# Kernel optimization log

Hardware: AMD Instinct MI355X
Metric: run time of the kernel (lower is better)

Reference implementation:

```python
import jax, jax.numpy as jnp
import numpy as np

N_USER = 100000
N_ITEM = 200000
N_NODES = N_USER + N_ITEM
NNZ = 4000000
EMB = 64
N_LAYERS = 3
BATCH = 4096


def setup_inputs() -> dict:
    key = jax.random.key(0)
    ks = jax.random.split(key, 12)
    inp = {
        'users': jax.random.randint(ks[0], (BATCH,), 0, N_USER, dtype=jnp.int32),
        'pos_items': jax.random.randint(ks[1], (BATCH,), 0, N_ITEM, dtype=jnp.int32),
        'neg_items': jax.random.randint(ks[2], (BATCH,), 0, N_ITEM, dtype=jnp.int32),
        'row': jax.random.randint(ks[3], (NNZ,), 0, N_NODES, dtype=jnp.int32),
        'col': jax.random.randint(ks[4], (NNZ,), 0, N_NODES, dtype=jnp.int32),
        'vals': jax.random.uniform(ks[5], (NNZ,), dtype=jnp.float32),
        'user_emb': 0.1 * jax.random.normal(ks[6], (N_USER, EMB), dtype=jnp.float32),
        'item_emb': 0.1 * jax.random.normal(ks[7], (N_ITEM, EMB), dtype=jnp.float32),
        'W_gc': 0.1 * jax.random.normal(ks[8], (N_LAYERS, EMB, EMB), dtype=jnp.float32),
        'b_gc': 0.1 * jax.random.normal(ks[9], (N_LAYERS, EMB), dtype=jnp.float32),
        'W_bi': 0.1 * jax.random.normal(ks[10], (N_LAYERS, EMB, EMB), dtype=jnp.float32),
        'b_bi': 0.1 * jax.random.normal(ks[11], (N_LAYERS, EMB), dtype=jnp.float32),
    }
    return inp


def _l2_normalize(x, eps=1e-12):
    # matches torch F.normalize(p=2, dim=1): x / max(||x||, eps)
    n = jnp.sqrt(jnp.sum(x * x, axis=1, keepdims=True))
    return x / jnp.maximum(n, eps)


def reference(users, pos_items, neg_items, row, col, vals, user_emb, item_emb, W_gc, b_gc, W_bi, b_bi):
    B = users.shape[0]
    # sparse adjacency propagation: side = A_hat @ [user_emb; item_emb]
    emb = jnp.concatenate([user_emb, item_emb], axis=0)          # [N, d]
    msgs = vals[:, None] * emb[col]                               # [nnz, d]
    side = jax.ops.segment_sum(msgs, row, num_segments=N_NODES)  # [N, d]

    u_side = side[users]                                          # [B, d]
    i_side = jnp.concatenate([side[N_USER + pos_items], side[N_USER + neg_items]], axis=0)
    small_side = jnp.concatenate([u_side, i_side], axis=0)        # [3B, d]
    ego = jnp.concatenate([user_emb[users], item_emb[pos_items], item_emb[neg_items]], axis=0)

    all_embeddings = [ego]
    for k in range(N_LAYERS):
        sum_e = small_side @ W_gc[k] + b_gc[k]
        bi = (ego * small_side) @ W_bi[k] + b_bi[k]
        ego = jax.nn.leaky_relu(sum_e + bi, negative_slope=0.2)
        all_embeddings.append(_l2_normalize(ego))

    all_e = jnp.concatenate(all_embeddings, axis=1)               # [3B, d*(L+1)]
    u_g = all_e[:B]
    i_g = all_e[B:]
    pos_g = i_g[:B]
    neg_g = i_g[B:]
    return (u_g, pos_g, neg_g)
```

## Files before the change

kernel.cpp:

```cpp
#include <hip/hip_runtime.h>

#define N_USER   100000
#define N_ITEM   200000
#define N_NODES  300000
#define NNZ      4000000
#define EMB      64
#define N_LAYERS 3
#define BATCH    4096
#define NSLOT    (3*BATCH)
#define MAXE     96


__global__ void k_setup(const int* __restrict__ users,
                        const int* __restrict__ pos,
                        const int* __restrict__ neg,
                        int* __restrict__ slot_of_node,
                        int* __restrict__ count) {
    int i = blockIdx.x * blockDim.x + threadIdx.x;
    if (i >= NSLOT) return;
    count[i] = 0;
    int node;
    if (i < BATCH)            node = users[i];
    else if (i < 2 * BATCH)   node = N_USER + pos[i - BATCH];
    else                      node = N_USER + neg[i - 2 * BATCH];
    slot_of_node[node] = i;
}

__global__ void __launch_bounds__(256) k_build(
        const int* __restrict__ row,
        const int* __restrict__ col,
        const float* __restrict__ vals,
        const int* __restrict__ slot_of_node,
        int* __restrict__ count,
        int* __restrict__ csr_col,
        float* __restrict__ csr_val) {
    int stride = gridDim.x * blockDim.x;
    for (int e = blockIdx.x * blockDim.x + threadIdx.x; e < NNZ; e += stride) {
        int s = slot_of_node[row[e]];
        if (s >= 0) {
            int p = atomicAdd(&count[s], 1);
            if (p < MAXE) {
                csr_col[(size_t)s * MAXE + p] = col[e];
                csr_val[(size_t)s * MAXE + p] = vals[e];
            }
        }
    }
}

__global__ void __launch_bounds__(256) k_gather_mlp(
        const int* __restrict__ users,
        const int* __restrict__ pos,
        const int* __restrict__ neg,
        const float* __restrict__ user_emb,
        const float* __restrict__ item_emb,
        const float* __restrict__ W_gc,
        const float* __restrict__ b_gc,
        const float* __restrict__ W_bi,
        const float* __restrict__ b_bi,
        const int* __restrict__ slot_of_node,
        const int* __restrict__ count,
        const int* __restrict__ csr_col,
        const float* __restrict__ csr_val,
        float* __restrict__ out) {
    __shared__ float s_lds[4][EMB];
    __shared__ float e_lds[4][EMB];
    int w = threadIdx.x >> 6;
    int j = threadIdx.x & 63;
    int slot = blockIdx.x * 4 + w;

    int node;
    if (slot < BATCH)          node = users[slot];
    else if (slot < 2 * BATCH) node = N_USER + pos[slot - BATCH];
    else                       node = N_USER + neg[slot - 2 * BATCH];

    const float* erow = (node < N_USER) ? (user_emb + (size_t)node * EMB)
                                        : (item_emb + (size_t)(node - N_USER) * EMB);
    int wslot = slot_of_node[node];
    int n = count[wslot];
    n = (n < MAXE) ? n : MAXE;
    const int*   cc = csr_col + (size_t)wslot * MAXE;
    const float* cv = csr_val + (size_t)wslot * MAXE;

    float acc = 0.f;
    int t = 0;
    for (; t + 1 < n; t += 2) {
        int   c0 = cc[t],     c1 = cc[t + 1];
        float v0 = cv[t],     v1 = cv[t + 1];
        const float* s0 = (c0 < N_USER) ? (user_emb + (size_t)c0 * EMB)
                                        : (item_emb + (size_t)(c0 - N_USER) * EMB);
        const float* s1 = (c1 < N_USER) ? (user_emb + (size_t)c1 * EMB)
                                        : (item_emb + (size_t)(c1 - N_USER) * EMB);
        float g0 = s0[j];
        float g1 = s1[j];
        acc = fmaf(v0, g0, acc);
        acc = fmaf(v1, g1, acc);
    }
    if (t < n) {
        int   c0 = cc[t];
        float v0 = cv[t];
        const float* s0 = (c0 < N_USER) ? (user_emb + (size_t)c0 * EMB)
                                        : (item_emb + (size_t)(c0 - N_USER) * EMB);
        acc = fmaf(v0, s0[j], acc);
    }

    float e0 = erow[j];
    s_lds[w][j] = acc;
    e_lds[w][j] = e0;
    out[(size_t)slot * 256 + j] = e0;
    __syncthreads();

    for (int k = 0; k < N_LAYERS; ++k) {
        const float* wgc = W_gc + (size_t)k * EMB * EMB;
        const float* wbi = W_bi + (size_t)k * EMB * EMB;
        float sum1 = b_gc[k * EMB + j];
        float sum2 = b_bi[k * EMB + j];
        #pragma unroll 8
        for (int i = 0; i < EMB; ++i) {
            float si = s_lds[w][i];
            float pi = si * e_lds[w][i];
            sum1 = fmaf(si, wgc[i * EMB + j], sum1);
            sum2 = fmaf(pi, wbi[i * EMB + j], sum2);
        }
        float x = sum1 + sum2;
        x = (x >= 0.f) ? x : 0.2f * x;

        float sq = x * x;
        #pragma unroll
        for (int o = 32; o; o >>= 1) sq += __shfl_xor(sq, o, 64);
        float nn = fmaxf(sqrtf(sq), 1e-12f);
        out[(size_t)slot * 256 + (k + 1) * 64 + j] = x / nn;

        __syncthreads();
        e_lds[w][j] = x;
        __syncthreads();
    }
}

extern "C" void kernel_launch(void* const* d_in, const int* in_sizes, int n_in,
                              void* d_out, int out_size, void* d_ws, size_t ws_size,
                              hipStream_t stream) {
    const int*   users    = (const int*)  d_in[0];
    const int*   pos      = (const int*)  d_in[1];
    const int*   neg      = (const int*)  d_in[2];
    const int*   row      = (const int*)  d_in[3];
    const int*   col      = (const int*)  d_in[4];
    const float* vals     = (const float*)d_in[5];
    const float* user_emb = (const float*)d_in[6];
    const float* item_emb = (const float*)d_in[7];
    const float* W_gc     = (const float*)d_in[8];
    const float* b_gc     = (const float*)d_in[9];
    const float* W_bi     = (const float*)d_in[10];
    const float* b_bi     = (const float*)d_in[11];
    float* out = (float*)d_out;

    char* ws = (char*)d_ws;
    int*   slot_of_node = (int*)ws;
    int*   count        = (int*)(ws + 1200128);
    int*   csr_col      = (int*)(ws + 1249280);
    float* csr_val      = (float*)(ws + 5967872);

    hipMemsetAsync(slot_of_node, 0xFF, (size_t)N_NODES * sizeof(int), stream);

    k_setup<<<(NSLOT + 255) / 256, 256, 0, stream>>>(users, pos, neg,
                                                     slot_of_node, count);
    k_build<<<2048, 256, 0, stream>>>(row, col, vals, slot_of_node,
                                      count, csr_col, csr_val);
    k_gather_mlp<<<NSLOT / 4, 256, 0, stream>>>(users, pos, neg,
                                                user_emb, item_emb,
                                                W_gc, b_gc, W_bi, b_bi,
                                                slot_of_node, count,
                                                csr_col, csr_val, out);
}
```

Before: 92.15 us.

## Vectorize edge scan, stage MLP weights in LDS, batch neighbor gathers via shuffles

The build kernel now reads row indices as int4 with one thread per four edges, replacing the grid-stride loop. The gather/MLP kernel uses 512-thread blocks (8 slots each), loads each layer's W_gc and W_bi into shared memory, and broadcasts the per-slot vectors with wave shuffles instead of LDS arrays. Neighbor indices and values are fetched once per lane and broadcast by shuffle, with 16 gathers issued before their FMAs to expose memory-level parallelism. The risk is the per-layer weight reload and the block-wide syncs that add latency and LDS pressure (32KB per block), which may lower occupancy.

```diff
diff --git a/kernel.cpp b/kernel.cpp
--- a/kernel.cpp
+++ b/kernel.cpp
@@ -9,6 +9,8 @@
 #define BATCH    4096
 #define NSLOT    (3*BATCH)
 #define MAXE     96
+#define BDIM     512
+#define WPB      8
 
 
 __global__ void k_setup(const int* __restrict__ users,
@@ -34,20 +36,21 @@
         int* __restrict__ count,
         int* __restrict__ csr_col,
         float* __restrict__ csr_val) {
-    int stride = gridDim.x * blockDim.x;
-    for (int e = blockIdx.x * blockDim.x + threadIdx.x; e < NNZ; e += stride) {
-        int s = slot_of_node[row[e]];
-        if (s >= 0) {
-            int p = atomicAdd(&count[s], 1);
-            if (p < MAXE) {
-                csr_col[(size_t)s * MAXE + p] = col[e];
-                csr_val[(size_t)s * MAXE + p] = vals[e];
-            }
-        }
-    }
+    int t = blockIdx.x * blockDim.x + threadIdx.x;
+    if (t >= NNZ / 4) return;
+    int4 r = ((const int4*)row)[t];
+    int s0 = slot_of_node[r.x];
+    int s1 = slot_of_node[r.y];
+    int s2 = slot_of_node[r.z];
+    int s3 = slot_of_node[r.w];
+    int e = t * 4;
+    if (s0 >= 0) { int p = atomicAdd(&count[s0], 1); if (p < MAXE) { csr_col[(size_t)s0*MAXE+p] = col[e];   csr_val[(size_t)s0*MAXE+p] = vals[e];   } }
+    if (s1 >= 0) { int p = atomicAdd(&count[s1], 1); if (p < MAXE) { csr_col[(size_t)s1*MAXE+p] = col[e+1]; csr_val[(size_t)s1*MAXE+p] = vals[e+1]; } }
+    if (s2 >= 0) { int p = atomicAdd(&count[s2], 1); if (p < MAXE) { csr_col[(size_t)s2*MAXE+p] = col[e+2]; csr_val[(size_t)s2*MAXE+p] = vals[e+2]; } }
+    if (s3 >= 0) { int p = atomicAdd(&count[s3], 1); if (p < MAXE) { csr_col[(size_t)s3*MAXE+p] = col[e+3]; csr_val[(size_t)s3*MAXE+p] = vals[e+3]; } }
 }
 
-__global__ void __launch_bounds__(256) k_gather_mlp(
+__global__ void __launch_bounds__(BDIM) k_fused(
         const int* __restrict__ users,
         const int* __restrict__ pos,
         const int* __restrict__ neg,
@@ -62,11 +65,21 @@
         const int* __restrict__ csr_col,
         const float* __restrict__ csr_val,
         float* __restrict__ out) {
-    __shared__ float s_lds[4][EMB];
-    __shared__ float e_lds[4][EMB];
-    int w = threadIdx.x >> 6;
-    int j = threadIdx.x & 63;
-    int slot = blockIdx.x * 4 + w;
+    __shared__ float wg_lds[EMB * EMB];
+    __shared__ float wb_lds[EMB * EMB];
+    int tid = threadIdx.x;
+    int w = tid >> 6;
+    int j = tid & 63;
+    int slot = blockIdx.x * WPB + w;
+
+    {
+        const float4* g4 = (const float4*)W_gc;
+        const float4* b4 = (const float4*)W_bi;
+        float4* lg = (float4*)wg_lds;
+        float4* lb = (float4*)wb_lds;
+        #pragma unroll
+        for (int i = tid; i < EMB * EMB / 4; i += BDIM) { lg[i] = g4[i]; lb[i] = b4[i]; }
+    }
 
     int node;
     if (slot < BATCH)          node = users[slot];
@@ -81,45 +94,48 @@
     const int*   cc = csr_col + (size_t)wslot * MAXE;
     const float* cv = csr_val + (size_t)wslot * MAXE;
 
-    float acc = 0.f;
-    int t = 0;
-    for (; t + 1 < n; t += 2) {
-        int   c0 = cc[t],     c1 = cc[t + 1];
-        float v0 = cv[t],     v1 = cv[t + 1];
-        const float* s0 = (c0 < N_USER) ? (user_emb + (size_t)c0 * EMB)
-                                        : (item_emb + (size_t)(c0 - N_USER) * EMB);
-        const float* s1 = (c1 < N_USER) ? (user_emb + (size_t)c1 * EMB)
-                                        : (item_emb + (size_t)(c1 - N_USER) * EMB);
-        float g0 = s0[j];
-        float g1 = s1[j];
-        acc = fmaf(v0, g0, acc);
-        acc = fmaf(v1, g1, acc);
+    int   cj = (j < n) ? cc[j] : 0;
+    float vj = (j < n) ? cv[j] : 0.f;
+
+    float sval = 0.f;
+    int nmain = (n < 64) ? n : 64;
+    for (int t0 = 0; t0 < nmain; t0 += 16) {
+        float gg[16], vv[16];
+        #pragma unroll
+        for (int k = 0; k < 16; ++k) {
+            int t = (t0 + k) & 63;
+            int   c = __shfl(cj, t, 64);
+            float v = __shfl(vj, t, 64);
+            const float* s = (c < N_USER) ? (user_emb + (size_t)c * EMB)
+                                          : (item_emb + (size_t)(c - N_USER) * EMB);
+            gg[k] = s[j];
+            vv[k] = v;
+        }
+        #pragma unroll
+        for (int k = 0; k < 16; ++k) sval = fmaf(vv[k], gg[k], sval);
     }
-    if (t < n) {
-        int   c0 = cc[t];
-        float v0 = cv[t];
-        const float* s0 = (c0 < N_USER) ? (user_emb + (size_t)c0 * EMB)
-                                        : (item_emb + (size_t)(c0 - N_USER) * EMB);
-        acc = fmaf(v0, s0[j], acc);
+    for (int t = 64; t < n; ++t) {
+        int c = cc[t];
+        float v = cv[t];
+        const float* s = (c < N_USER) ? (user_emb + (size_t)c * EMB)
+                                      : (item_emb + (size_t)(c - N_USER) * EMB);
+        sval = fmaf(v, s[j], sval);
     }
 
-    float e0 = erow[j];
-    s_lds[w][j] = acc;
-    e_lds[w][j] = e0;
-    out[(size_t)slot * 256 + j] = e0;
+    float e = erow[j];
+    out[(size_t)slot * 256 + j] = e;
     __syncthreads();
 
     for (int k = 0; k < N_LAYERS; ++k) {
-        const float* wgc = W_gc + (size_t)k * EMB * EMB;
-        const float* wbi = W_bi + (size_t)k * EMB * EMB;
+        float pval = sval * e;
         float sum1 = b_gc[k * EMB + j];
         float sum2 = b_bi[k * EMB + j];
-        #pragma unroll 8
+        #pragma unroll
         for (int i = 0; i < EMB; ++i) {
-            float si = s_lds[w][i];
-            float pi = si * e_lds[w][i];
-            sum1 = fmaf(si, wgc[i * EMB + j], sum1);
-            sum2 = fmaf(pi, wbi[i * EMB + j], sum2);
+            float si = __shfl(sval, i, 64);
+            float pi = __shfl(pval, i, 64);
+            sum1 = fmaf(si, wg_lds[i * EMB + j], sum1);
+            sum2 = fmaf(pi, wb_lds[i * EMB + j], sum2);
         }
         float x = sum1 + sum2;
         x = (x >= 0.f) ? x : 0.2f * x;
@@ -129,10 +145,18 @@
         for (int o = 32; o; o >>= 1) sq += __shfl_xor(sq, o, 64);
         float nn = fmaxf(sqrtf(sq), 1e-12f);
         out[(size_t)slot * 256 + (k + 1) * 64 + j] = x / nn;
+        e = x;
 
-        __syncthreads();
-        e_lds[w][j] = x;
-        __syncthreads();
+        if (k + 1 < N_LAYERS) {
+            __syncthreads();
+            const float4* g4 = (const float4*)(W_gc + (size_t)(k + 1) * EMB * EMB);
+            const float4* b4 = (const float4*)(W_bi + (size_t)(k + 1) * EMB * EMB);
+            float4* lg = (float4*)wg_lds;
+            float4* lb = (float4*)wb_lds;
+            #pragma unroll
+            for (int i2 = tid; i2 < EMB * EMB / 4; i2 += BDIM) { lg[i2] = g4[i2]; lb[i2] = b4[i2]; }
+            __syncthreads();
+        }
     }
 }
 
@@ -163,11 +187,11 @@
 
     k_setup<<<(NSLOT + 255) / 256, 256, 0, stream>>>(users, pos, neg,
                                                      slot_of_node, count);
-    k_build<<<2048, 256, 0, stream>>>(row, col, vals, slot_of_node,
-                                      count, csr_col, csr_val);
-    k_gather_mlp<<<NSLOT / 4, 256, 0, stream>>>(users, pos, neg,
-                                                user_emb, item_emb,
-                                                W_gc, b_gc, W_bi, b_bi,
-                                                slot_of_node, count,
-                                                csr_col, csr_val, out);
+    k_build<<<(NNZ / 4 + 255) / 256, 256, 0, stream>>>(row, col, vals, slot_of_node,
+                                                       count, csr_col, csr_val);
+    k_fused<<<NSLOT / WPB, BDIM, 0, stream>>>(users, pos, neg,
+                                              user_emb, item_emb,
+                                              W_gc, b_gc, W_bi, b_bi,
+                                              slot_of_node, count,
+                                              csr_col, csr_val, out);
 }
```

After: 124.9 us. 35.5% more time.
